# Performance work log

Hardware: AMD Instinct MI355X
Metric: run time of the kernel (lower is better)

The kernel has to match this reference:

```python
import jax, jax.numpy as jnp
import numpy as np

N, D = 8192, 512
HEADS, DIM_HEAD, M, ITERS = 8, 64, 256, 6
WP = 256          # CustomAttention weight_params_dim
E = 262144        # number of adjacency edges
K = 33            # residual depthwise conv kernel


def setup_inputs():
    key = jax.random.key(0)
    ks = jax.random.split(key, 12)
    inner = HEADS * DIM_HEAD
    xav = (6.0 / (D + WP)) ** 0.5
    return {
        "dense": jax.random.normal(ks[0], (N, D), jnp.float32),
        "adj_rows": jax.random.randint(ks[1], (E,), 0, N, dtype=jnp.int32),
        "adj_cols": jax.random.randint(ks[2], (E,), 0, N, dtype=jnp.int32),
        "adj_vals": jnp.ones((E,), jnp.float32),
        "wq": jax.random.uniform(ks[3], (D, WP), jnp.float32, -xav, xav),
        "wk": jax.random.uniform(ks[4], (D, WP), jnp.float32, -xav, xav),
        "w_qkv": jax.random.normal(ks[5], (3 * inner, D), jnp.float32) * D ** -0.5,
        "w_out": jax.random.normal(ks[6], (D, inner), jnp.float32) * inner ** -0.5,
        "b_out": jnp.zeros((D,), jnp.float32),
        "res_kernel": jax.random.normal(ks[7], (HEADS, 1, K, 1), jnp.float32) * 0.05,
        "wv_w": jax.random.normal(ks[8], (D, D), jnp.float32) * D ** -0.5,
        "wv_b": jnp.zeros((D,), jnp.float32),
    }


def _pinv(x, iters):
    # Moore-Penrose iterative pseudo-inverse (lucidrains nystrom-attention)
    ax = jnp.abs(x)
    z = jnp.swapaxes(x, -1, -2) / (ax.sum(-1).max() * ax.sum(-2).max())
    I = jnp.eye(x.shape[-1], dtype=x.dtype)
    for _ in range(iters):
        xz = x @ z
        z = 0.25 * z @ (13.0 * I - xz @ (15.0 * I - xz @ (7.0 * I - xz)))
    return z


def _nystrom(x, w_qkv, w_out, b_out, res_kernel):
    # x: [n, dim]; batch of 1 in original (squeezed here)
    n = x.shape[0]
    pad = (-n) % M
    xp = jnp.pad(x, ((pad, 0), (0, 0)))  # pad at front, as in original
    n_p = n + pad
    qkv = xp @ w_qkv.T  # [n_p, 3*h*d]
    q, k, v = [t.reshape(n_p, HEADS, DIM_HEAD).transpose(1, 0, 2)
               for t in jnp.split(qkv, 3, axis=-1)]  # each [h, n_p, d]
    q = q * DIM_HEAD ** -0.5
    l = n_p // M
    q_l = q.reshape(HEADS, M, l, DIM_HEAD).mean(2)  # [h, m, d] landmark means
    k_l = k.reshape(HEADS, M, l, DIM_HEAD).mean(2)
    a1 = jax.nn.softmax(jnp.einsum('hid,hjd->hij', q, k_l), -1)    # [h, n_p, m]
    a2 = jax.nn.softmax(jnp.einsum('hid,hjd->hij', q_l, k_l), -1)  # [h, m, m]
    a3 = jax.nn.softmax(jnp.einsum('hid,hjd->hij', q_l, k), -1)    # [h, m, n_p]
    out = (a1 @ _pinv(a2, ITERS)) @ (a3 @ v)  # [h, n_p, d]
    # residual depthwise conv over sequence dim, per head (groups=heads)
    res = jax.lax.conv_general_dilated(
        v[None], res_kernel, (1, 1), ((K // 2, K // 2), (0, 0)),
        dimension_numbers=('NCHW', 'OIHW', 'NCHW'), feature_group_count=HEADS)[0]
    out = out + res
    out = out.transpose(1, 0, 2).reshape(n_p, HEADS * DIM_HEAD) @ w_out.T + b_out
    return out[-n:]


def reference(dense, adj_rows, adj_cols, adj_vals, wq, wk, w_qkv, w_out, b_out,
              res_kernel, wv_w, wv_b):
    xg = _nystrom(dense, w_qkv, w_out, b_out, res_kernel)
    enc = xg + dense                              # [N, D]
    q = enc @ wq
    k = enc @ wk
    att = (q @ k.T) * (WP ** -0.5)                # [N, N] scaled logits
    # sparse adjacency mask + row-sum (torch.sparse.sum over dim=1)
    edge_scores = att[adj_rows, adj_cols] * adj_vals
    A_raw = jax.ops.segment_sum(edge_scores, adj_rows, num_segments=dense.shape[0])
    alpha = jax.nn.softmax(A_raw)                 # softmax over all N instances
    value = dense @ wv_w.T + wv_b                 # [N, D]
    xl = alpha[:, None] * value
    wei = jax.nn.sigmoid(-xl)
    sq = wei * wei
    xo = xl * 2.0 * sq + 2.0 * enc * (1.0 - sq)   # gated residual blend
    return xo, A_raw
```

## Files before the change

kernel.cpp:

```cpp
#include <hip/hip_runtime.h>
#include <hip/hip_bf16.h>

#define NSEQ 8192
#define DDIM 512
#define HEADS 8
#define DH 64
#define MLM 256
#define LSUB 32
#define WP 256
#define KCONV 33
#define INNER 512
#define QKV_LD 1536

static const size_t OFF_QKVBF  = 0;
static const size_t OFF_VT     = 6291456;
static const size_t OFF_SC     = 8388608;
#define PS (8388608)
static const size_t A2R_H = PS + 0;
static const size_t Z0R_H = PS + 524288;
static const size_t Z0T_H = PS + 1048576;
static const size_t Z1R_H = PS + 1572864;
static const size_t Z1T_H = PS + 2097152;
static const size_t PR_H  = PS + 2621440;
static const size_t PT_H  = PS + 3145728;
static const size_t T1T_H = PS + 3670016;
static const size_t T2T_H = PS + 4194304;
static const size_t A3VT_H= PS + 4718592;
static const size_t A2F32 = PS + 4849664;
static const size_t OFF_ATTNBF = 16777216;
static const size_t OFF_PART   = 18874368;
static const size_t OFF_ENC    = 0;
static const size_t OFF_ENCBF  = 4194304;
static const size_t OFF_QKE    = 6291456;
static const size_t OFF_DENSEBF= 20971520;
static const size_t OFF_WQKVBF = 23068672;
static const size_t OFF_WOUTBF = 23461888;
static const size_t OFF_WQKT   = 23592960;
static const size_t OFF_WVBF   = 23724032;
static const size_t OFF_QL     = 23855104;
static const size_t OFF_KL     = 23986176;
static const size_t OFF_QLBF   = 24117248;
static const size_t OFF_KLSBF  = 24182784;
static const size_t OFF_BBT    = 24248320;
static const size_t OFF_SCAL   = 24313856;
static const size_t OFF_ALPHA  = 24313872;
static const size_t OFF_DEN3   = 24322064;

__device__ __forceinline__ float bf2f(unsigned short u) {
    return __uint_as_float(((unsigned int)u) << 16);
}
__device__ __forceinline__ unsigned short f2bf(float x) {
    unsigned int u = __float_as_uint(x);
    u += 0x7FFFu + ((u >> 16) & 1u);
    return (unsigned short)(u >> 16);
}

typedef __attribute__((ext_vector_type(8))) short bf16x8;
typedef __attribute__((ext_vector_type(4))) float f32x4;

__device__ __forceinline__ void gload_lds16(const void* g, void* l) {
    __builtin_amdgcn_global_load_lds(
        (const __attribute__((address_space(1))) unsigned int*)g,
        (__attribute__((address_space(3))) unsigned int*)l, 16, 0, 0);
}

__global__ __launch_bounds__(256) void cvt_bf16_k(
    const float* __restrict__ in, unsigned short* __restrict__ out)
{
    size_t i = ((size_t)blockIdx.x * 256 + threadIdx.x) * 8;
    float4 a = *reinterpret_cast<const float4*>(in + i);
    float4 b = *reinterpret_cast<const float4*>(in + i + 4);
    uint4 p;
    p.x = (unsigned int)f2bf(a.x) | ((unsigned int)f2bf(a.y) << 16);
    p.y = (unsigned int)f2bf(a.z) | ((unsigned int)f2bf(a.w) << 16);
    p.z = (unsigned int)f2bf(b.x) | ((unsigned int)f2bf(b.y) << 16);
    p.w = (unsigned int)f2bf(b.z) | ((unsigned int)f2bf(b.w) << 16);
    *reinterpret_cast<uint4*>(out + i) = p;
}

__global__ __launch_bounds__(256) void tcvt_bf16_k(
    const float* __restrict__ in, unsigned short* __restrict__ out, int R, int C)
{
    int idx = blockIdx.x * 256 + threadIdx.x;
    if (idx < R * C) {
        int oc = idx / R;
        int orow = idx % R;
        out[idx] = f2bf(in[(size_t)orow * C + oc]);
    }
}

__global__ __launch_bounds__(256) void gemm_mfma_ntb(
    const unsigned short* __restrict__ A, int lda, size_t sA,
    const unsigned short* __restrict__ B, int ldb, size_t sB,
    float* __restrict__ C, unsigned short* __restrict__ Cbf, int ldc, size_t sC,
    int K, const float* __restrict__ bias, const float* __restrict__ addsrc,
    const float* __restrict__ alphav, float* __restrict__ denv, int epi)
{
    __shared__ __align__(16) unsigned short As[64 * 64];
    __shared__ __align__(16) unsigned short Bs[128 * 64];
    const int tid = threadIdx.x;
    const int wave = tid >> 6, lane = tid & 63;
    const int l15 = lane & 15, l4 = lane >> 4;
    const int wm = wave >> 1, wn = wave & 1;
    const size_t bm = (size_t)blockIdx.x * 64;
    const size_t bn = (size_t)blockIdx.y * 128;
    const int z = blockIdx.z;
    const unsigned short* Ab = A + (size_t)z * sA;
    const unsigned short* Bb = B + (size_t)z * sB;
    const int swzr = (l15 & 7) << 3;
    f32x4 acc[2][4] = {};
    for (int k0 = 0; k0 < K; k0 += 64) {
        __syncthreads();
#pragma unroll
        for (int c2 = 0; c2 < 2; ++c2) {
            int id = c2 * 256 + tid;
            int row = id >> 3;
            int cg = ((id & 7) ^ (row & 7)) << 3;
            gload_lds16(Ab + (bm + row) * (size_t)lda + k0 + cg, As + id * 8);
        }
#pragma unroll
        for (int c2 = 0; c2 < 4; ++c2) {
            int id = c2 * 256 + tid;
            int row = id >> 3;
            int cg = ((id & 7) ^ (row & 7)) << 3;
            gload_lds16(Bb + (bn + row) * (size_t)ldb + k0 + cg, Bs + id * 8);
        }
        __syncthreads();
#pragma unroll
        for (int c = 0; c < 2; ++c) {
            bf16x8 af[2], bfv[4];
#pragma unroll
            for (int i = 0; i < 2; ++i)
                af[i] = *reinterpret_cast<const bf16x8*>(
                    &As[(wm * 32 + i * 16 + l15) * 64 + ((c * 32 + l4 * 8) ^ swzr)]);
#pragma unroll
            for (int j = 0; j < 4; ++j)
                bfv[j] = *reinterpret_cast<const bf16x8*>(
                    &Bs[(wn * 64 + j * 16 + l15) * 64 + ((c * 32 + l4 * 8) ^ swzr)]);
#pragma unroll
            for (int i = 0; i < 2; ++i)
#pragma unroll
                for (int j = 0; j < 4; ++j)
                    acc[i][j] = __builtin_amdgcn_mfma_f32_16x16x32_bf16(
                        af[i], bfv[j], acc[i][j], 0, 0, 0);
        }
    }
    float* Cz = C ? C + (size_t)z * sC : nullptr;
    unsigned short* Cbz = Cbf ? Cbf + (size_t)z * sC : nullptr;
    if (epi == 3) {
#pragma unroll
        for (int i = 0; i < 2; ++i)
#pragma unroll
            for (int r = 0; r < 4; ++r) {
                size_t row = bm + wm * 32 + i * 16 + l4 * 4 + r;
                float s = 0.f;
#pragma unroll
                for (int j = 0; j < 4; ++j) {
                    size_t col = bn + wn * 64 + j * 16 + l15;
                    float e = __expf(acc[i][j][r]);
                    s += e;
                    Cbz[row * (size_t)ldc + col] = f2bf(e);
                }
                s += __shfl_xor(s, 1); s += __shfl_xor(s, 2);
                s += __shfl_xor(s, 4); s += __shfl_xor(s, 8);
                if (l15 == 0) atomicAdd(denv + (size_t)z * MLM + row, s);
            }
        return;
    }
#pragma unroll
    for (int i = 0; i < 2; ++i)
#pragma unroll
        for (int j = 0; j < 4; ++j)
#pragma unroll
            for (int r = 0; r < 4; ++r) {
                size_t row = bm + wm * 32 + i * 16 + l4 * 4 + r;
                size_t col = bn + wn * 64 + j * 16 + l15;
                float v = acc[i][j][r];
                if (bias) v += bias[col];
                if (epi == 2) {
                    float xl = alphav[row] * v;
                    float w = 1.f / (1.f + __expf(xl));
                    float sq = w * w;
                    v = xl * 2.f * sq + 2.f * addsrc[row * (size_t)ldc + col] * (1.f - sq);
                    Cz[row * (size_t)ldc + col] = v;
                } else {
                    if (addsrc) v += addsrc[row * (size_t)ldc + col];
                    if (epi == 1) v = __expf(v);
                    if (Cz)  Cz[row * (size_t)ldc + col] = v;
                    if (Cbz) Cbz[row * (size_t)ldc + col] = f2bf(v);
                }
            }
}

__global__ __launch_bounds__(256) void bmm_h(
    const unsigned short* __restrict__ Ah, const unsigned short* __restrict__ Bh,
    unsigned short* __restrict__ Crh, unsigned short* __restrict__ Cth,
    int M, int N, int K, int ntn, float alpha, float beta)
{
    __shared__ __align__(16) unsigned short LAh[64 * 64];
    __shared__ __align__(16) unsigned short LBh[64 * 64];
    const int tid = threadIdx.x;
    const int wave = tid >> 6, lane = tid & 63;
    const int l15 = lane & 15, l4 = lane >> 4;
    const int wm = wave >> 1, wn = wave & 1;
    const int b = blockIdx.y;
    const int tm = blockIdx.x / ntn, tn = blockIdx.x % ntn;
    const unsigned short* Ahb = Ah + (size_t)b * M * K;
    const unsigned short* Bhb = Bh + (size_t)b * N * K;
    const int swzr = (l15 & 7) << 3;
    f32x4 acc[2][2] = {};
    for (int k0 = 0; k0 < K; k0 += 64) {
        __syncthreads();
#pragma unroll
        for (int c2 = 0; c2 < 2; ++c2) {
            int id = c2 * 256 + tid;
            int row = id >> 3;
            int cg = ((id & 7) ^ (row & 7)) << 3;
            gload_lds16(Ahb + (size_t)(tm * 64 + row) * K + k0 + cg, LAh + id * 8);
            gload_lds16(Bhb + (size_t)(tn * 64 + row) * K + k0 + cg, LBh + id * 8);
        }
        __syncthreads();
#pragma unroll
        for (int c = 0; c < 2; ++c) {
            bf16x8 ah[2], bh[2];
#pragma unroll
            for (int i = 0; i < 2; ++i)
                ah[i] = *reinterpret_cast<const bf16x8*>(
                    &LAh[(wm * 32 + i * 16 + l15) * 64 + ((c * 32 + l4 * 8) ^ swzr)]);
#pragma unroll
            for (int j = 0; j < 2; ++j)
                bh[j] = *reinterpret_cast<const bf16x8*>(
                    &LBh[(wn * 32 + j * 16 + l15) * 64 + ((c * 32 + l4 * 8) ^ swzr)]);
#pragma unroll
            for (int i = 0; i < 2; ++i)
#pragma unroll
                for (int j = 0; j < 2; ++j)
                    acc[i][j] = __builtin_amdgcn_mfma_f32_16x16x32_bf16(ah[i], bh[j], acc[i][j], 0, 0, 0);
        }
    }
    unsigned short* Crhb = Crh ? Crh + (size_t)b * M * N : nullptr;
    unsigned short* Cthb = Cth ? Cth + (size_t)b * M * N : nullptr;
#pragma unroll
    for (int i = 0; i < 2; ++i)
#pragma unroll
        for (int j = 0; j < 2; ++j)
#pragma unroll
            for (int r = 0; r < 4; ++r) {
                int row = tm * 64 + wm * 32 + i * 16 + l4 * 4 + r;
                int col = tn * 64 + wn * 32 + j * 16 + l15;
                float v = beta * acc[i][j][r];
                if (alpha != 0.f)
                    v += alpha * bf2f(Ahb[(size_t)row * K + col]);
                unsigned short hi = f2bf(v);
                if (Crhb) Crhb[(size_t)row * N + col] = hi;
                if (Cthb) Cthb[(size_t)col * M + row] = hi;
            }
}

__global__ __launch_bounds__(256) void pv3_mfma(
    const unsigned short* __restrict__ sc, const unsigned short* __restrict__ vT,
    float* __restrict__ part)
{
    __shared__ __align__(16) unsigned short As[64 * 64];
    __shared__ __align__(16) unsigned short Bs[64 * 64];
    const int tid = threadIdx.x;
    const int wave = tid >> 6, lane = tid & 63;
    const int l15 = lane & 15, l4 = lane >> 4;
    const int wm = wave >> 1, wn = wave & 1;
    const int it = blockIdx.x, kc = blockIdx.y, h = blockIdx.z;
    const unsigned short* Ap = sc + (size_t)h * MLM * NSEQ + (size_t)(it * 64) * NSEQ + kc * 512;
    const unsigned short* Bp = vT + (size_t)h * DH * NSEQ + kc * 512;
    const int swzr = (l15 & 7) << 3;
    f32x4 acc[2][2] = {};
    for (int k0 = 0; k0 < 512; k0 += 64) {
        __syncthreads();
#pragma unroll
        for (int c2 = 0; c2 < 2; ++c2) {
            int id = c2 * 256 + tid;
            int row = id >> 3;
            int cg = ((id & 7) ^ (row & 7)) << 3;
            gload_lds16(Ap + (size_t)row * NSEQ + k0 + cg, As + id * 8);
        }
#pragma unroll
        for (int c2 = 0; c2 < 2; ++c2) {
            int id = c2 * 256 + tid;
            int row = id >> 3;
            int cg = ((id & 7) ^ (row & 7)) << 3;
            gload_lds16(Bp + (size_t)row * NSEQ + k0 + cg, Bs + id * 8);
        }
        __syncthreads();
#pragma unroll
        for (int ks = 0; ks < 2; ++ks) {
            bf16x8 af[2], bfv[2];
#pragma unroll
            for (int i = 0; i < 2; ++i)
                af[i] = *reinterpret_cast<const bf16x8*>(
                    &As[(wm * 32 + i * 16 + l15) * 64 + ((ks * 32 + l4 * 8) ^ swzr)]);
#pragma unroll
            for (int j = 0; j < 2; ++j)
                bfv[j] = *reinterpret_cast<const bf16x8*>(
                    &Bs[(wn * 32 + j * 16 + l15) * 64 + ((ks * 32 + l4 * 8) ^ swzr)]);
#pragma unroll
            for (int i = 0; i < 2; ++i)
#pragma unroll
                for (int j = 0; j < 2; ++j)
                    acc[i][j] = __builtin_amdgcn_mfma_f32_16x16x32_bf16(af[i], bfv[j], acc[i][j], 0, 0, 0);
        }
    }
    float* Cp = part + ((size_t)(kc * 8 + h) * MLM + it * 64) * DH;
#pragma unroll
    for (int i = 0; i < 2; ++i)
#pragma unroll
        for (int j = 0; j < 2; ++j)
#pragma unroll
            for (int r = 0; r < 4; ++r)
                Cp[(wm * 32 + i * 16 + l4 * 4 + r) * DH + wn * 32 + j * 16 + l15] = acc[i][j][r];
}

__global__ __launch_bounds__(256) void a1_fused(
    const unsigned short* __restrict__ qkvbf,
    const unsigned short* __restrict__ kls,
    const unsigned short* __restrict__ bbT,
    const float* __restrict__ kern,
    unsigned short* __restrict__ attnbf)
{
    __shared__ __align__(16) unsigned short lds[16384];
    __shared__ float den[2][64];
    __shared__ float kc_s[KCONV];
    const int tid = threadIdx.x;
    const int wave = tid >> 6, lane = tid & 63;
    const int l15 = lane & 15, l4 = lane >> 4;
    const int wm = wave >> 1, wn = wave & 1;
    const int n0 = blockIdx.x * 64;
    const int h = blockIdx.y;
    const int swzr = (l15 & 7) << 3;

    if (tid < KCONV) kc_s[tid] = kern[h * KCONV + tid];
#pragma unroll
    for (int c2 = 0; c2 < 2; ++c2) {
        int id = c2 * 256 + tid;
        int row = id >> 3, cg = ((id & 7) ^ (row & 7)) << 3;
        gload_lds16(qkvbf + (size_t)(n0 + row) * QKV_LD + h * DH + cg, lds + id * 8);
    }
    __syncthreads();
    const unsigned short* klsh = kls + (size_t)h * (MLM * DH);
    f32x4 acc[2][8] = {};
#pragma unroll
    for (int c = 0; c < 2; ++c) {
        bf16x8 af[2], bv[8];
#pragma unroll
        for (int i = 0; i < 2; ++i) {
            int row = wm * 32 + i * 16 + l15;
            af[i] = *reinterpret_cast<const bf16x8*>(&lds[row * 64 + ((c * 32 + l4 * 8) ^ swzr)]);
        }
#pragma unroll
        for (int j = 0; j < 8; ++j) {
            int brow = wn * 128 + j * 16 + l15;
            bv[j] = *reinterpret_cast<const bf16x8*>(&klsh[brow * 64 + c * 32 + l4 * 8]);
        }
#pragma unroll
        for (int i = 0; i < 2; ++i)
#pragma unroll
            for (int j = 0; j < 8; ++j)
                acc[i][j] = __builtin_amdgcn_mfma_f32_16x16x32_bf16(af[i], bv[j], acc[i][j], 0, 0, 0);
    }
    __syncthreads();
    float rs[2][4] = {};
#pragma unroll
    for (int i = 0; i < 2; ++i)
#pragma unroll
        for (int j = 0; j < 8; ++j)
#pragma unroll
            for (int r = 0; r < 4; ++r) {
                float e = __expf(acc[i][j][r]);
                rs[i][r] += e;
                int row = wm * 32 + i * 16 + l4 * 4 + r;
                int col = wn * 128 + j * 16 + l15;
                lds[row * 256 + (col ^ ((row & 7) << 3))] = f2bf(e);
            }
#pragma unroll
    for (int i = 0; i < 2; ++i)
#pragma unroll
        for (int r = 0; r < 4; ++r) {
            float s = rs[i][r];
            s += __shfl_xor(s, 1); s += __shfl_xor(s, 2);
            s += __shfl_xor(s, 4); s += __shfl_xor(s, 8);
            if (l15 == 0) den[wn][wm * 32 + i * 16 + l4 * 4 + r] = s;
        }
    __syncthreads();
    f32x4 acc2[2][2] = {};
    const unsigned short* bbh = bbT + (size_t)h * DH * MLM;
#pragma unroll
    for (int k0 = 0; k0 < 256; k0 += 32) {
        bf16x8 af2[2], bv2[2];
#pragma unroll
        for (int i = 0; i < 2; ++i) {
            int row = wm * 32 + i * 16 + l15;
            af2[i] = *reinterpret_cast<const bf16x8*>(
                &lds[row * 256 + ((k0 + l4 * 8) ^ ((row & 7) << 3))]);
        }
#pragma unroll
        for (int j = 0; j < 2; ++j) {
            int d = wn * 32 + j * 16 + l15;
            bv2[j] = *reinterpret_cast<const bf16x8*>(&bbh[d * MLM + k0 + l4 * 8]);
        }
#pragma unroll
        for (int i = 0; i < 2; ++i)
#pragma unroll
            for (int j = 0; j < 2; ++j)
                acc2[i][j] = __builtin_amdgcn_mfma_f32_16x16x32_bf16(af2[i], bv2[j], acc2[i][j], 0, 0, 0);
    }
    __syncthreads();
    float* att = reinterpret_cast<float*>(lds);
    unsigned short* vbuf = &lds[8192];
#pragma unroll
    for (int i = 0; i < 2; ++i)
#pragma unroll
        for (int r = 0; r < 4; ++r) {
            int row = wm * 32 + i * 16 + l4 * 4 + r;
            float inv = 1.f / (den[0][row] + den[1][row]);
#pragma unroll
            for (int j = 0; j < 2; ++j)
                att[row * 64 + wn * 32 + j * 16 + l15] = acc2[i][j][r] * inv;
        }
#pragma unroll
    for (int s = 0; s < 6; ++s) {
        int id = s * 256 + tid;
        int r = id >> 4, c4 = (id & 15) * 4;
        int n = n0 - 16 + r;
        ushort4 u = {0, 0, 0, 0};
        if (n >= 0 && n < NSEQ)
            u = *reinterpret_cast<const ushort4*>(qkvbf + (size_t)n * QKV_LD + 1024 + h * 64 + c4);
        *reinterpret_cast<ushort4*>(vbuf + r * 64 + c4) = u;
    }
    __syncthreads();
    const int col = tid & 63, rowg = tid >> 6;
    float vwin[48];
#pragma unroll
    for (int t = 0; t < 48; ++t) vwin[t] = bf2f(vbuf[(rowg * 16 + t) * 64 + col]);
#pragma unroll
    for (int rr = 0; rr < 16; ++rr) {
        float cv = 0.f;
#pragma unroll
        for (int t = 0; t < KCONV; ++t) cv += kc_s[t] * vwin[rr + t];
        int row = rowg * 16 + rr;
        attnbf[(size_t)(n0 + row) * INNER + h * DH + col] = f2bf(att[row * 64 + col] + cv);
    }
}

__global__ __launch_bounds__(64) void landmark2_k(
    const unsigned short* __restrict__ qkvbf, float* __restrict__ q_l, float* __restrict__ k_l,
    unsigned short* __restrict__ ql_bf, unsigned short* __restrict__ kls_bf)
{
    int m = blockIdx.x, h = blockIdx.y, d = threadIdx.x;
    float sq = 0.f, sk = 0.f;
    for (int i = 0; i < LSUB; ++i) {
        size_t n = (size_t)m * LSUB + i;
        sq += bf2f(qkvbf[n * QKV_LD + h * DH + d]);
        sk += bf2f(qkvbf[n * QKV_LD + 512 + h * DH + d]);
    }
    float qv = sq * (0.125f / (float)LSUB);
    float kv = sk * (1.f / (float)LSUB);
    size_t o = ((size_t)h * MLM + m) * DH + d;
    q_l[o] = qv; k_l[o] = kv;
    ql_bf[o] = f2bf(qv);
    kls_bf[o] = f2bf(kv * 0.125f);
}

__global__ __launch_bounds__(256) void vt_k(
    const unsigned short* __restrict__ qkvbf, unsigned short* __restrict__ vT)
{
    __shared__ unsigned short tile[128][72];
    const int t = threadIdx.x;
    const int n0 = blockIdx.x * 128;
    const int h = blockIdx.y;
#pragma unroll
    for (int s = 0; s < 4; ++s) {
        int cid = s * 256 + t;
        int row = cid >> 3, ch = (cid & 7) * 8;
        uint4 v = *reinterpret_cast<const uint4*>(
            qkvbf + (size_t)(n0 + row) * QKV_LD + 1024 + h * 64 + ch);
        *reinterpret_cast<uint4*>(&tile[row][ch]) = v;
    }
    __syncthreads();
#pragma unroll
    for (int s = 0; s < 4; ++s) {
        int cid = s * 256 + t;
        int d = cid >> 4, nch = (cid & 15) * 8;
        unsigned short o[8];
#pragma unroll
        for (int i = 0; i < 8; ++i) o[i] = tile[nch + i][d];
        *reinterpret_cast<uint4*>(vT + (size_t)h * DH * NSEQ + (size_t)d * NSEQ + n0 + nch) =
            *reinterpret_cast<uint4*>(o);
    }
}

__global__ __launch_bounds__(256) void a2_k(
    const float* __restrict__ q_l, const float* __restrict__ k_l, float* __restrict__ a2)
{
    int i = blockIdx.x, h = blockIdx.y, t = threadIdx.x;
    __shared__ float ql[64];
    __shared__ float red[256];
    if (t < 64) ql[t] = q_l[((size_t)h * MLM + i) * DH + t];
    __syncthreads();
    const float* kr = k_l + ((size_t)h * MLM + t) * DH;
    float s = 0.f;
#pragma unroll
    for (int d = 0; d < 64; d += 4) {
        float4 kv = *reinterpret_cast<const float4*>(kr + d);
        s += kv.x * ql[d] + kv.y * ql[d + 1] + kv.z * ql[d + 2] + kv.w * ql[d + 3];
    }
    red[t] = s; __syncthreads();
    for (int off = 128; off > 0; off >>= 1) { if (t < off) red[t] = fmaxf(red[t], red[t + off]); __syncthreads(); }
    float m = red[0]; __syncthreads();
    float e = __expf(s - m);
    red[t] = e; __syncthreads();
    for (int off = 128; off > 0; off >>= 1) { if (t < off) red[t] += red[t + off]; __syncthreads(); }
    a2[(((size_t)h * MLM + i) * MLM) + t] = e / red[0];
}

__global__ __launch_bounds__(256) void absmax_k(
    const float* __restrict__ a2, unsigned int* __restrict__ scal)
{
    int b = blockIdx.x, t = threadIdx.x;
    __shared__ float red[256];
    float sum = 0.f;
    if (b < 8) {
        const float* r = a2 + ((size_t)b * MLM + t) * MLM;
        for (int j = 0; j < MLM; ++j) sum += fabsf(r[j]);
    } else {
        int h = b - 8;
        for (int i = 0; i < MLM; ++i) sum += fabsf(a2[((size_t)h * MLM + i) * MLM + t]);
    }
    red[t] = sum; __syncthreads();
    for (int off = 128; off > 0; off >>= 1) { if (t < off) red[t] = fmaxf(red[t], red[t + off]); __syncthreads(); }
    if (t == 0) atomicMax(scal + (b < 8 ? 0 : 1), __float_as_uint(red[0]));
}

__global__ __launch_bounds__(256) void zinit2_k(
    const float* __restrict__ a2, const unsigned int* __restrict__ scal,
    unsigned short* __restrict__ a2h,
    unsigned short* __restrict__ zrh, unsigned short* __restrict__ zth)
{
    int idx = blockIdx.x * 256 + threadIdx.x;
    float inv = 1.f / (__uint_as_float(scal[0]) * __uint_as_float(scal[1]));
    int h = idx >> 16, rem = idx & 65535, i = rem >> 8, j = rem & 255;
    float aij = a2[idx];
    a2h[idx] = f2bf(aij);
    zth[idx] = f2bf(aij * inv);
    zrh[idx] = f2bf(a2[((size_t)h << 16) + (j << 8) + i] * inv);
}

__global__ __launch_bounds__(256) void red3_k(
    const float* __restrict__ part, const float* __restrict__ den3,
    unsigned short* __restrict__ a3vth)
{
    int o = blockIdx.x * 256 + threadIdx.x;
    float s = 0.f;
#pragma unroll
    for (int kc = 0; kc < 16; ++kc) s += part[(size_t)kc * 131072 + o];
    s /= den3[o >> 6];
    int h = o >> 14, i = (o >> 6) & 255, d = o & 63;
    a3vth[(h << 14) + (d << 8) + i] = f2bf(s);
}

__global__ __launch_bounds__(256) void edge2_k(
    const unsigned short* __restrict__ qke,
    const int* __restrict__ rows, const int* __restrict__ cols,
    const float* __restrict__ vals, float* __restrict__ A_raw)
{
    const int e = blockIdx.x * 32 + (threadIdx.x >> 3);
    const int g = threadIdx.x & 7;
    const int r = rows[e], c = cols[e];
    const unsigned short* qr = qke + (size_t)r * 512 + g * 32;
    const unsigned short* kr = qke + (size_t)c * 512 + 256 + g * 32;
    float s = 0.f;
#pragma unroll
    for (int u = 0; u < 4; ++u) {
        uint4 qa = *reinterpret_cast<const uint4*>(qr + u * 8);
        uint4 ka = *reinterpret_cast<const uint4*>(kr + u * 8);
        unsigned int qw[4] = {qa.x, qa.y, qa.z, qa.w};
        unsigned int kw[4] = {ka.x, ka.y, ka.z, ka.w};
#pragma unroll
        for (int q = 0; q < 4; ++q) {
            s += bf2f((unsigned short)(qw[q] & 0xFFFF)) * bf2f((unsigned short)(kw[q] & 0xFFFF));
            s += bf2f((unsigned short)(qw[q] >> 16)) * bf2f((unsigned short)(kw[q] >> 16));
        }
    }
    s += __shfl_xor(s, 1); s += __shfl_xor(s, 2); s += __shfl_xor(s, 4);
    if (g == 0) atomicAdd(&A_raw[r], s * vals[e] * 0.0625f);
}

__global__ __launch_bounds__(1024) void alpha_k(
    const float* __restrict__ A_raw, float* __restrict__ alpha)
{
    __shared__ float red[1024];
    int t = threadIdx.x;
    float m = -1e30f;
    for (int i = t; i < NSEQ; i += 1024) m = fmaxf(m, A_raw[i]);
    red[t] = m; __syncthreads();
    for (int off = 512; off > 0; off >>= 1) { if (t < off) red[t] = fmaxf(red[t], red[t + off]); __syncthreads(); }
    m = red[0]; __syncthreads();
    float s = 0.f;
    for (int i = t; i < NSEQ; i += 1024) s += __expf(A_raw[i] - m);
    red[t] = s; __syncthreads();
    for (int off = 512; off > 0; off >>= 1) { if (t < off) red[t] += red[t + off]; __syncthreads(); }
    float inv = 1.f / red[0];
    for (int i = t; i < NSEQ; i += 1024) alpha[i] = __expf(A_raw[i] - m) * inv;
}

extern "C" void kernel_launch(void* const* d_in, const int* in_sizes, int n_in,
                              void* d_out, int out_size, void* d_ws, size_t ws_size,
                              hipStream_t stream)
{
    const float* dense      = (const float*)d_in[0];
    const int*   adj_rows   = (const int*)d_in[1];
    const int*   adj_cols   = (const int*)d_in[2];
    const float* adj_vals   = (const float*)d_in[3];
    const float* wq         = (const float*)d_in[4];
    const float* wk         = (const float*)d_in[5];
    const float* w_qkv      = (const float*)d_in[6];
    const float* w_out      = (const float*)d_in[7];
    const float* b_out      = (const float*)d_in[8];
    const float* res_kernel = (const float*)d_in[9];
    const float* wv_w       = (const float*)d_in[10];
    const float* wv_b       = (const float*)d_in[11];
    const int E = in_sizes[1];

    float* ws  = (float*)d_ws;
    float* out = (float*)d_out;
    float* A_raw = out + (size_t)NSEQ * DDIM;

    unsigned short* qkv_bf   = (unsigned short*)(ws + OFF_QKVBF);
    unsigned short* vT       = (unsigned short*)(ws + OFF_VT);
    unsigned short* sc       = (unsigned short*)(ws + OFF_SC);
    unsigned short* attn_bf  = (unsigned short*)(ws + OFF_ATTNBF);
    unsigned short* qke_bf   = (unsigned short*)(ws + OFF_QKE);
    unsigned short* dense_bf = (unsigned short*)(ws + OFF_DENSEBF);
    unsigned short* wqkv_bf  = (unsigned short*)(ws + OFF_WQKVBF);
    unsigned short* wout_bf  = (unsigned short*)(ws + OFF_WOUTBF);
    unsigned short* wqkT_bf  = (unsigned short*)(ws + OFF_WQKT);
    unsigned short* wv_bf    = (unsigned short*)(ws + OFF_WVBF);
    unsigned short* ql_bf    = (unsigned short*)(ws + OFF_QLBF);
    unsigned short* kls_bf   = (unsigned short*)(ws + OFF_KLSBF);
    unsigned short* bbT_bf   = (unsigned short*)(ws + OFF_BBT);
    unsigned short* enc_bf   = (unsigned short*)(ws + OFF_ENCBF);

#define U16(off) ((unsigned short*)(ws + (off)))

    (void)hipMemsetAsync(A_raw, 0, NSEQ * sizeof(float), stream);
    (void)hipMemsetAsync(ws + OFF_SCAL, 0, 2 * sizeof(unsigned int), stream);
    (void)hipMemsetAsync(ws + OFF_DEN3, 0, HEADS * MLM * sizeof(float), stream);

    cvt_bf16_k<<<(NSEQ * DDIM) / 2048, 256, 0, stream>>>(dense, dense_bf);
    cvt_bf16_k<<<(1536 * DDIM) / 2048, 256, 0, stream>>>(w_qkv, wqkv_bf);

    gemm_mfma_ntb<<<dim3(NSEQ / 64, 1536 / 128, 1), 256, 0, stream>>>(
        dense_bf, DDIM, 0, wqkv_bf, DDIM, 0, nullptr, qkv_bf, QKV_LD, 0,
        DDIM, nullptr, nullptr, nullptr, nullptr, 0);

    landmark2_k<<<dim3(MLM, HEADS), 64, 0, stream>>>(
        qkv_bf, ws + OFF_QL, ws + OFF_KL, ql_bf, kls_bf);
    vt_k<<<dim3(NSEQ / 128, HEADS), 256, 0, stream>>>(qkv_bf, vT);

    gemm_mfma_ntb<<<dim3(MLM / 64, NSEQ / 128, HEADS), 256, 0, stream>>>(
        ql_bf, DH, (size_t)MLM * DH, qkv_bf + 512, QKV_LD, DH,
        nullptr, sc, NSEQ, (size_t)MLM * NSEQ, DH, nullptr, nullptr, nullptr,
        ws + OFF_DEN3, 3);
    pv3_mfma<<<dim3(4, 16, HEADS), 256, 0, stream>>>(sc, vT, ws + OFF_PART);
    red3_k<<<512, 256, 0, stream>>>(ws + OFF_PART, ws + OFF_DEN3, U16(A3VT_H));

    a2_k<<<dim3(MLM, HEADS), 256, 0, stream>>>(ws + OFF_QL, ws + OFF_KL, ws + A2F32);
    absmax_k<<<16, 256, 0, stream>>>(ws + A2F32, (unsigned int*)(ws + OFF_SCAL));
    zinit2_k<<<(HEADS * MLM * MLM) / 256, 256, 0, stream>>>(
        ws + A2F32, (const unsigned int*)(ws + OFF_SCAL),
        U16(A2R_H), U16(Z0R_H), U16(Z0T_H));

    for (int it = 0; it < 6; ++it) {
        size_t zr_h = (it & 1) ? Z1R_H : Z0R_H;
        size_t zt_h = (it & 1) ? Z1T_H : Z0T_H;
        size_t or_h = (it & 1) ? Z0R_H : Z1R_H;
        size_t ot_h = (it & 1) ? Z0T_H : Z1T_H;
        bmm_h<<<dim3(16, HEADS), 256, 0, stream>>>(
            U16(A2R_H), U16(zt_h), U16(PR_H), U16(PT_H), 256, 256, 256, 4, 0.f, 1.f);
        bmm_h<<<dim3(16, HEADS), 256, 0, stream>>>(
            U16(PR_H), U16(PT_H), nullptr, U16(T1T_H), 256, 256, 256, 4, 7.f, -1.f);
        bmm_h<<<dim3(16, HEADS), 256, 0, stream>>>(
            U16(PR_H), U16(T1T_H), nullptr, U16(T2T_H), 256, 256, 256, 4, 15.f, -1.f);
        bmm_h<<<dim3(16, HEADS), 256, 0, stream>>>(
            U16(zr_h), U16(T2T_H), U16(or_h), U16(ot_h), 256, 256, 256, 4, 3.25f, -0.25f);
    }
    bmm_h<<<dim3(4, HEADS), 256, 0, stream>>>(
        U16(A3VT_H), U16(Z0R_H), bbT_bf, nullptr, 64, 256, 256, 4, 0.f, 1.f);

    a1_fused<<<dim3(NSEQ / 64, HEADS), 256, 0, stream>>>(
        qkv_bf, kls_bf, bbT_bf, res_kernel, attn_bf);

    cvt_bf16_k<<<(DDIM * INNER) / 2048, 256, 0, stream>>>(w_out, wout_bf);
    tcvt_bf16_k<<<(WP * DDIM + 255) / 256, 256, 0, stream>>>(wq, wqkT_bf, DDIM, WP);
    tcvt_bf16_k<<<(WP * DDIM + 255) / 256, 256, 0, stream>>>(wk, wqkT_bf + 256 * 512, DDIM, WP);
    cvt_bf16_k<<<(DDIM * DDIM) / 2048, 256, 0, stream>>>(wv_w, wv_bf);

    gemm_mfma_ntb<<<dim3(NSEQ / 64, DDIM / 128, 1), 256, 0, stream>>>(
        attn_bf, INNER, 0, wout_bf, INNER, 0, ws + OFF_ENC, enc_bf, DDIM, 0,
        INNER, b_out, dense, nullptr, nullptr, 0);

    gemm_mfma_ntb<<<dim3(NSEQ / 64, 512 / 128, 1), 256, 0, stream>>>(
        enc_bf, DDIM, 0, wqkT_bf, DDIM, 0, nullptr, qke_bf, 512, 0,
        DDIM, nullptr, nullptr, nullptr, nullptr, 0);

    edge2_k<<<E / 32, 256, 0, stream>>>(qke_bf, adj_rows, adj_cols, adj_vals, A_raw);
    alpha_k<<<1, 1024, 0, stream>>>(A_raw, ws + OFF_ALPHA);

    gemm_mfma_ntb<<<dim3(NSEQ / 64, DDIM / 128, 1), 256, 0, stream>>>(
        dense_bf, DDIM, 0, wv_bf, DDIM, 0, out, nullptr, DDIM, 0,
        DDIM, wv_b, ws + OFF_ENC, ws + OFF_ALPHA, nullptr, 2);
}
```

Baseline: 502.4 us.

## Fuse pseudo-inverse iteration chain into one persistent kernel per head

Replaces the 25 separate small batched-matmul launches of the Moore-Penrose iteration with a single kernel that runs one 1024-thread block per head. Stages are separated by threadfence plus block barriers. Operands are read straight from global memory (L2) instead of being staged through LDS. The transposed output is written as vectorised ushort4 stores. This removes launch overhead and inter-kernel gaps, but uses only 8 blocks on a GPU with many CUs, so per-stage throughput drops.

Result: slower. 1.666 ms (+231.6%).

```diff
diff --git a/kernel.cpp b/kernel.cpp
--- a/kernel.cpp
+++ b/kernel.cpp
@@ -192,69 +192,88 @@
             }
 }
 
-__global__ __launch_bounds__(256) void bmm_h(
-    const unsigned short* __restrict__ Ah, const unsigned short* __restrict__ Bh,
-    unsigned short* __restrict__ Crh, unsigned short* __restrict__ Cth,
-    int M, int N, int K, int ntn, float alpha, float beta)
-{
-    __shared__ __align__(16) unsigned short LAh[64 * 64];
-    __shared__ __align__(16) unsigned short LBh[64 * 64];
-    const int tid = threadIdx.x;
-    const int wave = tid >> 6, lane = tid & 63;
-    const int l15 = lane & 15, l4 = lane >> 4;
-    const int wm = wave >> 1, wn = wave & 1;
-    const int b = blockIdx.y;
-    const int tm = blockIdx.x / ntn, tn = blockIdx.x % ntn;
-    const unsigned short* Ahb = Ah + (size_t)b * M * K;
-    const unsigned short* Bhb = Bh + (size_t)b * N * K;
-    const int swzr = (l15 & 7) << 3;
-    f32x4 acc[2][2] = {};
-    for (int k0 = 0; k0 < K; k0 += 64) {
-        __syncthreads();
-#pragma unroll
-        for (int c2 = 0; c2 < 2; ++c2) {
-            int id = c2 * 256 + tid;
-            int row = id >> 3;
-            int cg = ((id & 7) ^ (row & 7)) << 3;
-            gload_lds16(Ahb + (size_t)(tm * 64 + row) * K + k0 + cg, LAh + id * 8);
-            gload_lds16(Bhb + (size_t)(tn * 64 + row) * K + k0 + cg, LBh + id * 8);
-        }
-        __syncthreads();
-#pragma unroll
-        for (int c = 0; c < 2; ++c) {
-            bf16x8 ah[2], bh[2];
-#pragma unroll
-            for (int i = 0; i < 2; ++i)
-                ah[i] = *reinterpret_cast<const bf16x8*>(
-                    &LAh[(wm * 32 + i * 16 + l15) * 64 + ((c * 32 + l4 * 8) ^ swzr)]);
-#pragma unroll
-            for (int j = 0; j < 2; ++j)
-                bh[j] = *reinterpret_cast<const bf16x8*>(
-                    &LBh[(wn * 32 + j * 16 + l15) * 64 + ((c * 32 + l4 * 8) ^ swzr)]);
-#pragma unroll
-            for (int i = 0; i < 2; ++i)
-#pragma unroll
-                for (int j = 0; j < 2; ++j)
-                    acc[i][j] = __builtin_amdgcn_mfma_f32_16x16x32_bf16(ah[i], bh[j], acc[i][j], 0, 0, 0);
-        }
-    }
-    unsigned short* Crhb = Crh ? Crh + (size_t)b * M * N : nullptr;
-    unsigned short* Cthb = Cth ? Cth + (size_t)b * M * N : nullptr;
-#pragma unroll
-    for (int i = 0; i < 2; ++i)
-#pragma unroll
-        for (int j = 0; j < 2; ++j)
+__device__ __forceinline__ void pinv_stage(
+    const unsigned short* __restrict__ A,
+    const unsigned short* __restrict__ Bt,
+    unsigned short* __restrict__ Cr,
+    unsigned short* __restrict__ Ct,
+    float alpha, float beta,
+    int wm, int wn, int l15, int l4)
+{
+    f32x4 acc[4][4] = {};
+    for (int k0 = 0; k0 < 256; k0 += 32) {
+        bf16x8 af[4], bf[4];
+#pragma unroll
+        for (int i = 0; i < 4; ++i)
+            af[i] = *reinterpret_cast<const bf16x8*>(
+                &A[(size_t)(wm * 64 + i * 16 + l15) * 256 + k0 + l4 * 8]);
+#pragma unroll
+        for (int j = 0; j < 4; ++j)
+            bf[j] = *reinterpret_cast<const bf16x8*>(
+                &Bt[(size_t)(wn * 64 + j * 16 + l15) * 256 + k0 + l4 * 8]);
+#pragma unroll
+        for (int i = 0; i < 4; ++i)
+#pragma unroll
+            for (int j = 0; j < 4; ++j)
+                acc[i][j] = __builtin_amdgcn_mfma_f32_16x16x32_bf16(
+                    af[i], bf[j], acc[i][j], 0, 0, 0);
+    }
+#pragma unroll
+    for (int i = 0; i < 4; ++i)
+#pragma unroll
+        for (int j = 0; j < 4; ++j) {
+            int row0 = wm * 64 + i * 16 + l4 * 4;
+            int col = wn * 64 + j * 16 + l15;
+            unsigned short hv[4];
 #pragma unroll
             for (int r = 0; r < 4; ++r) {
-                int row = tm * 64 + wm * 32 + i * 16 + l4 * 4 + r;
-                int col = tn * 64 + wn * 32 + j * 16 + l15;
                 float v = beta * acc[i][j][r];
                 if (alpha != 0.f)
-                    v += alpha * bf2f(Ahb[(size_t)row * K + col]);
-                unsigned short hi = f2bf(v);
-                if (Crhb) Crhb[(size_t)row * N + col] = hi;
-                if (Cthb) Cthb[(size_t)col * M + row] = hi;
+                    v += alpha * bf2f(A[(size_t)(row0 + r) * 256 + col]);
+                hv[r] = f2bf(v);
+                if (Cr) Cr[(size_t)(row0 + r) * 256 + col] = hv[r];
             }
+            if (Ct)
+                *reinterpret_cast<ushort4*>(&Ct[(size_t)col * 256 + row0]) =
+                    make_ushort4(hv[0], hv[1], hv[2], hv[3]);
+        }
+}
+
+__global__ __launch_bounds__(1024) void pinv_fused_k(
+    const unsigned short* __restrict__ a2r,
+    unsigned short* __restrict__ z0r, unsigned short* __restrict__ z0t,
+    unsigned short* __restrict__ z1r, unsigned short* __restrict__ z1t,
+    unsigned short* __restrict__ pr,  unsigned short* __restrict__ pt,
+    unsigned short* __restrict__ t1t, unsigned short* __restrict__ t2t,
+    const unsigned short* __restrict__ a3vt,
+    unsigned short* __restrict__ bbT)
+{
+    const size_t off = (size_t)blockIdx.x * 65536;
+    const int tid = threadIdx.x;
+    const int lane = tid & 63, wave = tid >> 6;
+    const int l15 = lane & 15, l4 = lane >> 4;
+    const int wm = wave >> 2, wn = wave & 3;
+#define PFENCE() do { __threadfence(); __syncthreads(); } while (0)
+#pragma unroll 1
+    for (int it = 0; it < 6; ++it) {
+        const unsigned short* zr = ((it & 1) ? z1r : z0r) + off;
+        const unsigned short* zt = ((it & 1) ? z1t : z0t) + off;
+        unsigned short* orr = ((it & 1) ? z0r : z1r) + off;
+        unsigned short* ot  = ((it & 1) ? z0t : z1t) + off;
+        pinv_stage(a2r + off, zt, pr + off, pt + off, 0.f, 1.f, wm, wn, l15, l4);
+        PFENCE();
+        pinv_stage(pr + off, pt + off, nullptr, t1t + off, 7.f, -1.f, wm, wn, l15, l4);
+        PFENCE();
+        pinv_stage(pr + off, t1t + off, nullptr, t2t + off, 15.f, -1.f, wm, wn, l15, l4);
+        PFENCE();
+        pinv_stage(zr, t2t + off, orr, ot, 3.25f, -0.25f, wm, wn, l15, l4);
+        PFENCE();
+    }
+    if (wm == 0)
+        pinv_stage(a3vt + (size_t)blockIdx.x * 16384, z0r + off,
+                   bbT + (size_t)blockIdx.x * 16384, nullptr, 0.f, 1.f,
+                   0, wn, l15, l4);
+#undef PFENCE
 }
 
 __global__ __launch_bounds__(256) void pv3_mfma(
@@ -676,22 +695,10 @@
         ws + A2F32, (const unsigned int*)(ws + OFF_SCAL),
         U16(A2R_H), U16(Z0R_H), U16(Z0T_H));
 
-    for (int it = 0; it < 6; ++it) {
-        size_t zr_h = (it & 1) ? Z1R_H : Z0R_H;
-        size_t zt_h = (it & 1) ? Z1T_H : Z0T_H;
-        size_t or_h = (it & 1) ? Z0R_H : Z1R_H;
-        size_t ot_h = (it & 1) ? Z0T_H : Z1T_H;
-        bmm_h<<<dim3(16, HEADS), 256, 0, stream>>>(
-            U16(A2R_H), U16(zt_h), U16(PR_H), U16(PT_H), 256, 256, 256, 4, 0.f, 1.f);
-        bmm_h<<<dim3(16, HEADS), 256, 0, stream>>>(
-            U16(PR_H), U16(PT_H), nullptr, U16(T1T_H), 256, 256, 256, 4, 7.f, -1.f);
-        bmm_h<<<dim3(16, HEADS), 256, 0, stream>>>(
-            U16(PR_H), U16(T1T_H), nullptr, U16(T2T_H), 256, 256, 256, 4, 15.f, -1.f);
-        bmm_h<<<dim3(16, HEADS), 256, 0, stream>>>(
-            U16(zr_h), U16(T2T_H), U16(or_h), U16(ot_h), 256, 256, 256, 4, 3.25f, -0.25f);
-    }
-    bmm_h<<<dim3(4, HEADS), 256, 0, stream>>>(
-        U16(A3VT_H), U16(Z0R_H), bbT_bf, nullptr, 64, 256, 256, 4, 0.f, 1.f);
+    pinv_fused_k<<<HEADS, 1024, 0, stream>>>(
+        U16(A2R_H), U16(Z0R_H), U16(Z0T_H), U16(Z1R_H), U16(Z1T_H),
+        U16(PR_H), U16(PT_H), U16(T1T_H), U16(T2T_H),
+        U16(A3VT_H), bbT_bf);
 
     a1_fused<<<dim3(NSEQ / 64, HEADS), 256, 0, stream>>>(
         qkv_bf, kls_bf, bbT_bf, res_kernel, attn_bf);
```
